# Optimization experiments

Hardware: AMD Instinct MI355X
Metric: run time of the kernel (lower is better)

Reference implementation:

```python
import jax, jax.numpy as jnp
import numpy as np

N_S, N_C, N_L = 100000, 20000, 5000
E_U, E_T = 2000000, 500000
D_S, D_C, D_L, H = 64, 32, 128, 128
N_LAYERS = 3  # num_layers=2 -> ModuleList holds 3 hetero layers


def _sage(h_src, h_dst, src_idx, dst_idx, W_self, W_neigh, b, n_dst):
    # DGL SAGEConv 'mean': fc_self(h_dst) + fc_neigh(mean of in-neighbor src feats) + bias
    summed = jax.ops.segment_sum(h_src[src_idx], dst_idx, num_segments=n_dst)  # [n_dst, d]
    deg = jax.ops.segment_sum(jnp.ones((src_idx.shape[0],), h_src.dtype), dst_idx, num_segments=n_dst)
    h_neigh = summed / jnp.maximum(deg, 1.0)[:, None]
    return h_dst @ W_self + h_neigh @ W_neigh + b


def setup_inputs() -> dict:
    key = jax.random.key(0)
    ks = jax.random.split(key, 24)
    s = 0.05
    inp = {
        'feat_student': jax.random.normal(ks[0], (N_S, D_S), jnp.float32),
        'feat_concept': jax.random.normal(ks[1], (N_C, D_C), jnp.float32),
        'feat_lecture': jax.random.normal(ks[2], (N_L, D_L), jnp.float32),
        'W_fs': jax.random.normal(ks[3], (D_S, H), jnp.float32) * s,
        'b_fs': jnp.zeros((H,), jnp.float32),
        'W_fc': jax.random.normal(ks[4], (D_C, H), jnp.float32) * s,
        'b_fc': jnp.zeros((H,), jnp.float32),
        'W_fl': jax.random.normal(ks[5], (D_L, H), jnp.float32) * s,
        'b_fl': jnp.zeros((H,), jnp.float32),
        # per-layer, per-relation SAGE params (all dims 128 so they stack)
        'W_self_u': jax.random.normal(ks[6], (N_LAYERS, H, H), jnp.float32) * s,
        'W_neigh_u': jax.random.normal(ks[7], (N_LAYERS, H, H), jnp.float32) * s,
        'b_u': jnp.zeros((N_LAYERS, H), jnp.float32),
        'W_self_t': jax.random.normal(ks[8], (N_LAYERS, H, H), jnp.float32) * s,
        'W_neigh_t': jax.random.normal(ks[9], (N_LAYERS, H, H), jnp.float32) * s,
        'b_t': jnp.zeros((N_LAYERS, H), jnp.float32),
        'und_src': jax.random.randint(ks[10], (E_U,), 0, N_S, jnp.int32),
        'und_dst': jax.random.randint(ks[11], (E_U,), 0, N_C, jnp.int32),
        'tea_src': jax.random.randint(ks[12], (E_T,), 0, N_L, jnp.int32),
        'tea_dst': jax.random.randint(ks[13], (E_T,), 0, N_C, jnp.int32),
    }
    return inp


def reference(feat_student, feat_concept, feat_lecture,
              W_fs, b_fs, W_fc, b_fc, W_fl, b_fl,
              W_self_u, W_neigh_u, b_u, W_self_t, W_neigh_t, b_t,
              und_src, und_dst, tea_src, tea_dst):
    # input projections per node type
    h_s = feat_student @ W_fs + b_fs
    h_c = feat_concept @ W_fc + b_fc
    h_l = feat_lecture @ W_fl + b_fl
    n_c = h_c.shape[0]
    for i in range(N_LAYERS):
        ou = _sage(h_s, h_c, und_src, und_dst, W_self_u[i], W_neigh_u[i], b_u[i], n_c)
        ot = _sage(h_l, h_c, tea_src, tea_dst, W_self_t[i], W_neigh_t[i], b_t[i], n_c)
        # HeteroGraphConv cross-relation aggregate: 'mean' on layer 0, default 'sum' after
        h_c = (ou + ot) * (0.5 if i == 0 else 1.0)
        if i != N_LAYERS - 1:
            h_c = jax.nn.relu(h_c)  # dropout is identity in eval mode
        # student/lecture are never destination types -> features pass through
    return h_c  # [N_C, 128] concept embeddings
```

## Files before the change

### kernel.cpp

```cpp
#include <hip/hip_runtime.h>
#include <hip/hip_bf16.h>
#include <cstdint>
#include <cstddef>

#define NS_ 100000
#define NC_ 20000
#define NL_ 5000
#define EU_ 2000000
#define ET_ 500000
#define H_  128

#define NBK_ 625
#define CHK_ 3908
#define UBLK_ 512
#define TBLK_ 128
#define CAPU_ 3600
#define CAPT_ 1024
#define SEDGE_ 3712

typedef __attribute__((ext_vector_type(8))) short bs8;
typedef __attribute__((ext_vector_type(4))) float f32x4;
typedef __attribute__((ext_vector_type(2))) float v2f;

__device__ inline short bf_rne(float f) {
    unsigned u = __float_as_uint(f);
    u = (u + 0x7fffu + ((u >> 16) & 1u)) >> 16;
    return (short)u;
}
__device__ inline unsigned pack_bf16x2(float a, float b) {
    return ((unsigned)(unsigned short)bf_rne(a)) |
           (((unsigned)(unsigned short)bf_rne(b)) << 16);
}
__device__ inline float bflo(unsigned w) { return __uint_as_float(w << 16); }
__device__ inline float bfhi(unsigned w) { return __uint_as_float(w & 0xffff0000u); }

#define B_SCU UBLK_
#define B_SCT TBLK_
#define B_CVT 512
#define B_PACK 480
#define B_BC 2
#define B_WFC 16
#define B_TOTAL (B_SCU + B_SCT + B_CVT + B_PACK + B_BC + B_WFC)

__global__ __launch_bounds__(256) void prep_fused_kernel(
    const int* __restrict__ und_dst, const int* __restrict__ und_src,
    const int* __restrict__ tea_dst, const int* __restrict__ tea_src,
    unsigned* __restrict__ gcurU, unsigned* __restrict__ gcurT,
    unsigned* __restrict__ binnedU, unsigned* __restrict__ binnedT,
    const float* __restrict__ feat_s, unsigned* __restrict__ fs8,
    const float* __restrict__ feat_l, unsigned* __restrict__ flb,
    const float* __restrict__ Wsu, const float* __restrict__ Wnu,
    const float* __restrict__ Wst, const float* __restrict__ Wnt,
    const float* __restrict__ W_fs, const float* __restrict__ W_fl,
    short* __restrict__ WpL,
    const float* __restrict__ bu, const float* __restrict__ bt,
    const float* __restrict__ b_fs, const float* __restrict__ b_fl,
    float* __restrict__ bc,
    const float* __restrict__ W_fc, short* __restrict__ WpC)
{
    __shared__ unsigned smem[9476];
    const int b = blockIdx.x;
    const int tid = threadIdx.x;

    if (b < B_SCU + B_SCT) {
        const bool isU = (b < B_SCU);
        const int blk = isU ? b : (b - B_SCU);
        const int nEdge = isU ? EU_ : ET_;
        const int* dstp = isU ? und_dst : tea_dst;
        const int* srcp = isU ? und_src : tea_src;
        unsigned* gcur = isU ? gcurU : gcurT;
        unsigned* binned = isU ? binnedU : binnedT;
        const unsigned cap = isU ? CAPU_ : CAPT_;
        unsigned* sed  = smem;
        unsigned* sed2 = smem + 3968;
        unsigned* cnt  = smem + 7936;
        unsigned* pre  = smem + 8704;
        unsigned* wsum = smem + 9472;
        for (int i = tid; i < 768; i += 256) cnt[i] = 0;
        __syncthreads();
        const int start = blk * CHK_;
        const int end = min(start + CHK_, nEdge);
        const int n = end - start;
        const int n4 = n >> 2;
        const int4* d4 = (const int4*)(dstp + start);
        const int4* s4 = (const int4*)(srcp + start);
        for (int i = tid; i < n4; i += 256) {
            int4 dv = d4[i];
            int4 sv = s4[i];
            unsigned k0 = (unsigned)dv.x >> 5, k1 = (unsigned)dv.y >> 5;
            unsigned k2 = (unsigned)dv.z >> 5, k3 = (unsigned)dv.w >> 5;
            sed[4 * i + 0] = (unsigned)sv.x | ((unsigned)(dv.x & 31) << 17) | (k0 << 22);
            sed[4 * i + 1] = (unsigned)sv.y | ((unsigned)(dv.y & 31) << 17) | (k1 << 22);
            sed[4 * i + 2] = (unsigned)sv.z | ((unsigned)(dv.z & 31) << 17) | (k2 << 22);
            sed[4 * i + 3] = (unsigned)sv.w | ((unsigned)(dv.w & 31) << 17) | (k3 << 22);
            atomicAdd(&cnt[k0], 1u);
            atomicAdd(&cnt[k1], 1u);
            atomicAdd(&cnt[k2], 1u);
            atomicAdd(&cnt[k3], 1u);
        }
        for (int i = (n4 << 2) + tid; i < n; i += 256) {
            int d = dstp[start + i];
            unsigned k = (unsigned)d >> 5;
            sed[i] = (unsigned)srcp[start + i] | ((unsigned)(d & 31) << 17) | (k << 22);
            atomicAdd(&cnt[k], 1u);
        }
        __syncthreads();
        unsigned c0 = cnt[3 * tid], c1 = cnt[3 * tid + 1], c2 = cnt[3 * tid + 2];
        unsigned s = c0 + c1 + c2;
        const int lane = tid & 63;
        const int wv = tid >> 6;
        unsigned v = s;
#pragma unroll
        for (int d = 1; d < 64; d <<= 1) {
            unsigned t = __shfl_up(v, d, 64);
            if (lane >= d) v += t;
        }
        if (lane == 63) wsum[wv] = v;
        __syncthreads();
        unsigned wo = 0;
        for (int w = 0; w < wv; w++) wo += wsum[w];
        unsigned excl = v - s + wo;
        pre[3 * tid] = excl;
        pre[3 * tid + 1] = excl + c0;
        pre[3 * tid + 2] = excl + c0 + c1;
        __syncthreads();
        for (int k = tid; k < NBK_; k += 256) {
            unsigned L = cnt[k];
            unsigned W = L ? atomicAdd(&gcur[k], L) : 0;
            if (W + L > cap) W = cap - L;
            cnt[k] = k * cap + W - pre[k];
        }
        __syncthreads();
        for (int i = tid; i < n; i += 256) {
            unsigned e = sed[i];
            unsigned pos = atomicAdd(&pre[e >> 22], 1u);
            sed2[pos] = e;
        }
        __syncthreads();
        for (int i = tid; i < n; i += 256) {
            unsigned e = sed2[i];
            binned[cnt[e >> 22] + i] = e & 0x3FFFFFu;
        }
    } else if (b < B_SCU + B_SCT + B_CVT) {
        int i = (b - B_SCU - B_SCT) * 256 + tid;
        const int stride = B_CVT * 256;
        const int nS = NS_ * 16;
        const int nTot = nS + NL_ * 64;
        for (; i < nTot; i += stride) {
            if (i < nS) {
                const float4 v = ((const float4*)feat_s)[i];
                unsigned r = __builtin_amdgcn_cvt_pk_fp8_f32(v.x, v.y, 0, false);
                r = __builtin_amdgcn_cvt_pk_fp8_f32(v.z, v.w, r, true);
                fs8[i] = r;
            } else {
                int j = i - nS;
                float2 v = ((const float2*)feat_l)[j];
                flb[j] = pack_bf16x2(v.x, v.y);
            }
        }
    } else if (b < B_SCU + B_SCT + B_CVT + B_PACK) {
        int i = (b - B_SCU - B_SCT - B_CVT) * 256 + tid;
        int j = i & 7;
        int lane = (i >> 3) & 63;
        int nt = (i >> 9) & 7;
        int ktAll = i >> 12;
        int l = ktAll / 10;
        int kt = ktAll - l * 10;
        int k = kt * 32 + (lane >> 4) * 8 + j;
        int n = nt * 16 + (lane & 15);
        const size_t WL = (size_t)l * H_ * H_;
        float v;
        if (k < 128) {
            v = Wsu[WL + k * H_ + n] + Wst[WL + k * H_ + n];
        } else if (k < 192) {
            int a = k - 128;
            v = 0.f;
            for (int t = 0; t < 128; t++) v += W_fs[a * H_ + t] * Wnu[WL + t * H_ + n];
        } else {
            int a = k - 192;
            v = 0.f;
            for (int t = 0; t < 128; t++) v += W_fl[a * H_ + t] * Wnt[WL + t * H_ + n];
        }
        WpL[i] = bf_rne(v);
    } else if (b < B_SCU + B_SCT + B_CVT + B_PACK + B_BC) {
        int i = (b - B_SCU - B_SCT - B_CVT - B_PACK) * 256 + tid;
        if (i < 3 * H_) {
            int l = i >> 7, c = i & 127;
            const size_t WL = (size_t)l * H_ * H_;
            float v = bu[i] + bt[i];
            for (int j2 = 0; j2 < 128; j2++)
                v += b_fs[j2] * Wnu[WL + j2 * H_ + c] + b_fl[j2] * Wnt[WL + j2 * H_ + c];
            bc[i] = v;
        }
    } else {
        int i = (b - (B_SCU + B_SCT + B_CVT + B_PACK + B_BC)) * 256 + tid;
        int j = i & 7;
        int lane = (i >> 3) & 63;
        int nt = (i >> 9) & 7;
        int k = (lane >> 4) * 8 + j;
        int n = nt * 16 + (lane & 15);
        WpC[i] = bf_rne(W_fc[k * H_ + n]);
    }
}

__global__ __launch_bounds__(256) void agg_kernel(
    const unsigned* __restrict__ gcurU, const unsigned* __restrict__ binnedU,
    const uint2* __restrict__ fs8, unsigned* __restrict__ aggFu,
    const unsigned* __restrict__ gcurT, const unsigned* __restrict__ binnedT,
    const uint4* __restrict__ flb4, unsigned* __restrict__ aggFt)
{
    __shared__ unsigned sedA[SEDGE_];
    __shared__ unsigned sedB[SEDGE_];
    __shared__ unsigned sh[32], soff[33], scur[32];
    const int b = blockIdx.x;
    const int tid = threadIdx.x;
    const bool isU = (b < NBK_);
    const int bb = isU ? b : (b - NBK_);
    const unsigned* binned = isU ? binnedU : binnedT;
    const unsigned cap = isU ? CAPU_ : CAPT_;
    const unsigned* base = binned + (size_t)bb * cap;
    const int n = min((int)(isU ? gcurU : gcurT)[bb], (int)cap);

    if (tid < 32) sh[tid] = 0;
    __syncthreads();
    const int n4 = n >> 2;
    for (int i = tid; i < n4; i += 256) {
        uint4 w = ((const uint4*)base)[i];
        sedA[4 * i + 0] = w.x; atomicAdd(&sh[(w.x >> 17) & 31], 1u);
        sedA[4 * i + 1] = w.y; atomicAdd(&sh[(w.y >> 17) & 31], 1u);
        sedA[4 * i + 2] = w.z; atomicAdd(&sh[(w.z >> 17) & 31], 1u);
        sedA[4 * i + 3] = w.w; atomicAdd(&sh[(w.w >> 17) & 31], 1u);
    }
    for (int i = (n4 << 2) + tid; i < n; i += 256) {
        unsigned e = base[i];
        sedA[i] = e;
        atomicAdd(&sh[(e >> 17) & 31], 1u);
    }
    __syncthreads();
    if (tid == 0) {
        unsigned r = 0;
        for (int j = 0; j < 32; j++) {
            unsigned v = sh[j];
            soff[j] = r;
            scur[j] = r;
            r += v;
        }
        soff[32] = r;
    }
    __syncthreads();
    for (int i = tid; i < n; i += 256) {
        unsigned e = sedA[i];
        unsigned pos = atomicAdd(&scur[(e >> 17) & 31], 1u);
        if (pos < SEDGE_) sedB[pos] = e & 0x1FFFFu;
    }
    __syncthreads();

    const int g = tid >> 3;
    const int sub = tid & 7;
    const int gs = (int)soff[g];
    const int ge = (int)min(soff[g + 1], (unsigned)SEDGE_);
    const int c = bb * 32 + g;
    const float inv = 1.f / (float)max(ge - gs, 1);

    if (isU) {
        float a[8];
#pragma unroll
        for (int i = 0; i < 8; i++) a[i] = 0.f;
        int e = gs;
        for (; e + 2 <= ge; e += 2) {
            unsigned s0 = sedB[e], s1 = sedB[e + 1];
            uint2 w0 = fs8[(size_t)s0 * 8 + sub];
            uint2 w1 = fs8[(size_t)s1 * 8 + sub];
            v2f p0 = __builtin_amdgcn_cvt_pk_f32_fp8(w0.x, false);
            v2f p1 = __builtin_amdgcn_cvt_pk_f32_fp8(w0.x, true);
            v2f p2 = __builtin_amdgcn_cvt_pk_f32_fp8(w0.y, false);
            v2f p3 = __builtin_amdgcn_cvt_pk_f32_fp8(w0.y, true);
            a[0] += p0.x; a[1] += p0.y; a[2] += p1.x; a[3] += p1.y;
            a[4] += p2.x; a[5] += p2.y; a[6] += p3.x; a[7] += p3.y;
            p0 = __builtin_amdgcn_cvt_pk_f32_fp8(w1.x, false);
            p1 = __builtin_amdgcn_cvt_pk_f32_fp8(w1.x, true);
            p2 = __builtin_amdgcn_cvt_pk_f32_fp8(w1.y, false);
            p3 = __builtin_amdgcn_cvt_pk_f32_fp8(w1.y, true);
            a[0] += p0.x; a[1] += p0.y; a[2] += p1.x; a[3] += p1.y;
            a[4] += p2.x; a[5] += p2.y; a[6] += p3.x; a[7] += p3.y;
        }
        if (e < ge) {
            uint2 w0 = fs8[(size_t)sedB[e] * 8 + sub];
            v2f p0 = __builtin_amdgcn_cvt_pk_f32_fp8(w0.x, false);
            v2f p1 = __builtin_amdgcn_cvt_pk_f32_fp8(w0.x, true);
            v2f p2 = __builtin_amdgcn_cvt_pk_f32_fp8(w0.y, false);
            v2f p3 = __builtin_amdgcn_cvt_pk_f32_fp8(w0.y, true);
            a[0] += p0.x; a[1] += p0.y; a[2] += p1.x; a[3] += p1.y;
            a[4] += p2.x; a[5] += p2.y; a[6] += p3.x; a[7] += p3.y;
        }
        uint4 o;
        o.x = pack_bf16x2(a[0] * inv, a[1] * inv);
        o.y = pack_bf16x2(a[2] * inv, a[3] * inv);
        o.z = pack_bf16x2(a[4] * inv, a[5] * inv);
        o.w = pack_bf16x2(a[6] * inv, a[7] * inv);
        ((uint4*)aggFu)[(size_t)c * 8 + sub] = o;
    } else {
        float a[16];
#pragma unroll
        for (int i = 0; i < 16; i++) a[i] = 0.f;
        for (int e = gs; e < ge; e++) {
            unsigned src = sedB[e];
            uint4 w0 = flb4[(size_t)src * 16 + sub * 2];
            uint4 w1 = flb4[(size_t)src * 16 + sub * 2 + 1];
            a[0] += bflo(w0.x); a[1] += bfhi(w0.x);
            a[2] += bflo(w0.y); a[3] += bfhi(w0.y);
            a[4] += bflo(w0.z); a[5] += bfhi(w0.z);
            a[6] += bflo(w0.w); a[7] += bfhi(w0.w);
            a[8]  += bflo(w1.x); a[9]  += bfhi(w1.x);
            a[10] += bflo(w1.y); a[11] += bfhi(w1.y);
            a[12] += bflo(w1.z); a[13] += bfhi(w1.z);
            a[14] += bflo(w1.w); a[15] += bfhi(w1.w);
        }
        uint4 o0, o1;
        o0.x = pack_bf16x2(a[0] * inv, a[1] * inv);
        o0.y = pack_bf16x2(a[2] * inv, a[3] * inv);
        o0.z = pack_bf16x2(a[4] * inv, a[5] * inv);
        o0.w = pack_bf16x2(a[6] * inv, a[7] * inv);
        o1.x = pack_bf16x2(a[8] * inv, a[9] * inv);
        o1.y = pack_bf16x2(a[10] * inv, a[11] * inv);
        o1.z = pack_bf16x2(a[12] * inv, a[13] * inv);
        o1.w = pack_bf16x2(a[14] * inv, a[15] * inv);
        ((uint4*)aggFt)[(size_t)c * 16 + sub * 2] = o0;
        ((uint4*)aggFt)[(size_t)c * 16 + sub * 2 + 1] = o1;
    }
}

__global__ __launch_bounds__(256) void layers_fused_kernel(
    const float* __restrict__ feat_c, const short* __restrict__ WpC,
    const float* __restrict__ b_fc,
    const unsigned* __restrict__ aggFu, const unsigned* __restrict__ aggFt,
    const short* __restrict__ WpL, const float* __restrict__ bc,
    float* __restrict__ out)
{
    __shared__ short lds[4][16 * 132];
    const int tid = threadIdx.x;
    const int lane = tid & 63;
    const int wv = tid >> 6;
    const int row0 = blockIdx.x * 64 + wv * 16;
    const int q = lane >> 4;
    const int m = lane & 15;
    const int rA = min(row0 + m, NC_ - 1);
    short* tile = lds[wv];

    bs8 fuF[2], ftF[4], hcF[4];
#pragma unroll
    for (int kt = 0; kt < 2; kt++)
        fuF[kt] = *(const bs8*)(aggFu + (size_t)rA * 32 + kt * 16 + q * 4);
#pragma unroll
    for (int kt = 0; kt < 4; kt++)
        ftF[kt] = *(const bs8*)(aggFt + (size_t)rA * 64 + kt * 16 + q * 4);

    f32x4 acc[8];
#pragma unroll
    for (int i = 0; i < 8; i++) acc[i] = (f32x4){0.f, 0.f, 0.f, 0.f};
    {
        const float* xp = feat_c + (size_t)rA * 32 + q * 8;
        float4 xa = *(const float4*)xp;
        float4 xb = *(const float4*)(xp + 4);
        bs8 af;
        af[0] = bf_rne(xa.x); af[1] = bf_rne(xa.y); af[2] = bf_rne(xa.z); af[3] = bf_rne(xa.w);
        af[4] = bf_rne(xb.x); af[5] = bf_rne(xb.y); af[6] = bf_rne(xb.z); af[7] = bf_rne(xb.w);
#pragma unroll
        for (int nt = 0; nt < 8; nt++) {
            bs8 bfr = *(const bs8*)(WpC + ((size_t)nt * 64 + lane) * 8);
            acc[nt] = __builtin_amdgcn_mfma_f32_16x16x32_bf16(af, bfr, acc[nt], 0, 0, 0);
        }
    }
#pragma unroll
    for (int nt = 0; nt < 8; nt++) {
        int col = nt * 16 + m;
        float bv = b_fc[col];
#pragma unroll
        for (int r = 0; r < 4; r++)
            tile[(q * 4 + r) * 132 + col] = bf_rne(acc[nt][r] + bv);
    }
#pragma unroll
    for (int kt = 0; kt < 4; kt++)
        hcF[kt] = *(const bs8*)(tile + m * 132 + kt * 32 + q * 8);

#pragma unroll
    for (int l = 0; l < 3; l++) {
#pragma unroll
        for (int i = 0; i < 8; i++) acc[i] = (f32x4){0.f, 0.f, 0.f, 0.f};
        const short* wl = WpL + (size_t)l * 40960;
#pragma unroll
        for (int kt = 0; kt < 10; kt++) {
            bs8 af = (kt < 4) ? hcF[kt] : ((kt < 6) ? fuF[kt - 4] : ftF[kt - 6]);
            const short* wp = wl + (size_t)kt * 4096;
#pragma unroll
            for (int nt = 0; nt < 8; nt++) {
                bs8 bfr = *(const bs8*)(wp + ((size_t)nt * 64 + lane) * 8);
                acc[nt] = __builtin_amdgcn_mfma_f32_16x16x32_bf16(af, bfr, acc[nt], 0, 0, 0);
            }
        }
        const float scale = (l == 0) ? 0.5f : 1.0f;
        const float* bl = bc + l * H_;
        if (l < 2) {
#pragma unroll
            for (int nt = 0; nt < 8; nt++) {
                int col = nt * 16 + m;
                float bv = bl[col];
#pragma unroll
                for (int r = 0; r < 4; r++)
                    tile[(q * 4 + r) * 132 + col] =
                        bf_rne(fmaxf((acc[nt][r] + bv) * scale, 0.f));
            }
#pragma unroll
            for (int kt = 0; kt < 4; kt++)
                hcF[kt] = *(const bs8*)(tile + m * 132 + kt * 32 + q * 8);
        } else {
#pragma unroll
            for (int nt = 0; nt < 8; nt++) {
                int col = nt * 16 + m;
                float bv = bl[col];
#pragma unroll
                for (int r = 0; r < 4; r++) {
                    int row = row0 + q * 4 + r;
                    if (row < NC_)
                        out[(size_t)row * H_ + col] = (acc[nt][r] + bv) * scale;
                }
            }
        }
    }
}

extern "C" void kernel_launch(void* const* d_in, const int* in_sizes, int n_in,
                              void* d_out, int out_size, void* d_ws, size_t ws_size,
                              hipStream_t stream)
{
    (void)in_sizes; (void)n_in; (void)out_size; (void)ws_size;
    const float* feat_s = (const float*)d_in[0];
    const float* feat_c = (const float*)d_in[1];
    const float* feat_l = (const float*)d_in[2];
    const float* W_fs = (const float*)d_in[3];
    const float* b_fs = (const float*)d_in[4];
    const float* W_fc = (const float*)d_in[5];
    const float* b_fc = (const float*)d_in[6];
    const float* W_fl = (const float*)d_in[7];
    const float* b_fl = (const float*)d_in[8];
    const float* W_self_u  = (const float*)d_in[9];
    const float* W_neigh_u = (const float*)d_in[10];
    const float* b_u = (const float*)d_in[11];
    const float* W_self_t  = (const float*)d_in[12];
    const float* W_neigh_t = (const float*)d_in[13];
    const float* b_t = (const float*)d_in[14];
    const int* und_src = (const int*)d_in[15];
    const int* und_dst = (const int*)d_in[16];
    const int* tea_src = (const int*)d_in[17];
    const int* tea_dst = (const int*)d_in[18];
    float* out = (float*)d_out;

    char* ws = (char*)d_ws;
    size_t o = 0;
    auto alloc = [&](size_t bytes) -> char* {
        char* p = ws + o;
        o += (bytes + 255) & ~(size_t)255;
        return p;
    };
    unsigned* fs8  = (unsigned*)alloc((size_t)NS_ * 16 * 4);
    unsigned* flb  = (unsigned*)alloc((size_t)NL_ * 64 * 4);
    unsigned* aggFu = (unsigned*)alloc((size_t)NC_ * 32 * 4);
    unsigned* aggFt = (unsigned*)alloc((size_t)NC_ * 64 * 4);
    short* WpL = (short*)alloc((size_t)3 * 10 * 8 * 64 * 8 * 2);
    short* WpC = (short*)alloc((size_t)8 * 64 * 8 * 2);
    float* bc  = (float*)alloc((size_t)3 * H_ * 4);
    unsigned* gcurU = (unsigned*)alloc((size_t)NBK_ * 4);
    unsigned* gcurT = (unsigned*)alloc((size_t)NBK_ * 4);
    unsigned* binnedU = (unsigned*)alloc((size_t)NBK_ * CAPU_ * 4);
    unsigned* binnedT = (unsigned*)alloc((size_t)NBK_ * CAPT_ * 4);

    hipMemsetAsync(gcurU, 0, (size_t)((char*)binnedU - (char*)gcurU), stream);

    prep_fused_kernel<<<B_TOTAL, 256, 0, stream>>>(
        und_dst, und_src, tea_dst, tea_src, gcurU, gcurT, binnedU, binnedT,
        feat_s, fs8, feat_l, flb,
        W_self_u, W_neigh_u, W_self_t, W_neigh_t, W_fs, W_fl, WpL,
        b_u, b_t, b_fs, b_fl, bc,
        W_fc, WpC);

    agg_kernel<<<2 * NBK_, 256, 0, stream>>>(
        gcurU, binnedU, (const uint2*)fs8, aggFu,
        gcurT, binnedT, (const uint4*)flb, aggFt);

    layers_fused_kernel<<<(NC_ + 63) / 64, 256, 0, stream>>>(
        feat_c, WpC, b_fc, aggFu, aggFt, WpL, bc, out);
}
```

Before: 218.1 us.

## Fuse neighbor aggregation into layer kernel via shared-memory tiles per bucket

Merges the aggregation kernel and the three-layer MFMA kernel into one kernel with one block per 32-concept bucket. The block first aggregates the student and lecture relations and writes the results as bf16 into shared memory, then the matmul stage reads them from there. This removes the global aggFu/aggFt round trip and one launch. The MFMA work is split across four waves by row and column group, which adds block-wide syncs. The prep kernel's edge-chunk size is halved, which doubles the scatter blocks and shrinks their shared memory. The fused kernel launches only 625 blocks, so parallelism and latency hiding drop compared with the 1250 plus 313 blocks before.

```diff
diff --git a/kernel.cpp b/kernel.cpp
--- a/kernel.cpp
+++ b/kernel.cpp
@@ -11,9 +11,9 @@
 #define H_  128
 
 #define NBK_ 625
-#define CHK_ 3908
-#define UBLK_ 512
-#define TBLK_ 128
+#define CHK_ 1956
+#define UBLK_ 1023
+#define TBLK_ 256
 #define CAPU_ 3600
 #define CAPT_ 1024
 #define SEDGE_ 3712
@@ -58,7 +58,7 @@
     float* __restrict__ bc,
     const float* __restrict__ W_fc, short* __restrict__ WpC)
 {
-    __shared__ unsigned smem[9476];
+    __shared__ unsigned smem[5508];
     const int b = blockIdx.x;
     const int tid = threadIdx.x;
 
@@ -72,15 +72,15 @@
         unsigned* binned = isU ? binnedU : binnedT;
         const unsigned cap = isU ? CAPU_ : CAPT_;
         unsigned* sed  = smem;
-        unsigned* sed2 = smem + 3968;
-        unsigned* cnt  = smem + 7936;
-        unsigned* pre  = smem + 8704;
-        unsigned* wsum = smem + 9472;
+        unsigned* sed2 = smem + 1984;
+        unsigned* cnt  = smem + 3968;
+        unsigned* pre  = smem + 4736;
+        unsigned* wsum = smem + 5504;
         for (int i = tid; i < 768; i += 256) cnt[i] = 0;
         __syncthreads();
         const int start = blk * CHK_;
         const int end = min(start + CHK_, nEdge);
-        const int n = end - start;
+        const int n = max(end - start, 0);
         const int n4 = n >> 2;
         const int4* d4 = (const int4*)(dstp + start);
         const int4* s4 = (const int4*)(srcp + start);
@@ -203,24 +203,31 @@
     }
 }
 
-__global__ __launch_bounds__(256) void agg_kernel(
-    const unsigned* __restrict__ gcurU, const unsigned* __restrict__ binnedU,
-    const uint2* __restrict__ fs8, unsigned* __restrict__ aggFu,
-    const unsigned* __restrict__ gcurT, const unsigned* __restrict__ binnedT,
-    const uint4* __restrict__ flb4, unsigned* __restrict__ aggFt)
+#define SEDA_OFF 0
+#define SEDB_OFF SEDGE_
+#define TU_OFF   (2 * SEDGE_)
+#define TT_OFF   (TU_OFF + 32 * 36)
+#define SH_OFF   (TT_OFF + 32 * 68)
+#define SOFF_OFF (SH_OFF + 32)
+#define SCUR_OFF (SOFF_OFF + 33)
+#define SMEM_TOT (SCUR_OFF + 32)
+
+template <bool ISU>
+__device__ inline void agg_bucket(
+    int bb, const unsigned* __restrict__ gcur, const unsigned* __restrict__ binned,
+    const uint2* __restrict__ fs8, const uint4* __restrict__ flb4,
+    unsigned* __restrict__ smem, int tid)
 {
-    __shared__ unsigned sedA[SEDGE_];
-    __shared__ unsigned sedB[SEDGE_];
-    __shared__ unsigned sh[32], soff[33], scur[32];
-    const int b = blockIdx.x;
-    const int tid = threadIdx.x;
-    const bool isU = (b < NBK_);
-    const int bb = isU ? b : (b - NBK_);
-    const unsigned* binned = isU ? binnedU : binnedT;
-    const unsigned cap = isU ? CAPU_ : CAPT_;
+    unsigned* sedA = smem + SEDA_OFF;
+    unsigned* sedB = smem + SEDB_OFF;
+    unsigned* sh   = smem + SH_OFF;
+    unsigned* soff = smem + SOFF_OFF;
+    unsigned* scur = smem + SCUR_OFF;
+    const unsigned cap = ISU ? CAPU_ : CAPT_;
     const unsigned* base = binned + (size_t)bb * cap;
-    const int n = min((int)(isU ? gcurU : gcurT)[bb], (int)cap);
-
+    const int n = min((int)gcur[bb], (int)cap);
+
+    __syncthreads();
     if (tid < 32) sh[tid] = 0;
     __syncthreads();
     const int n4 = n >> 2;
@@ -259,10 +266,9 @@
     const int sub = tid & 7;
     const int gs = (int)soff[g];
     const int ge = (int)min(soff[g + 1], (unsigned)SEDGE_);
-    const int c = bb * 32 + g;
     const float inv = 1.f / (float)max(ge - gs, 1);
 
-    if (isU) {
+    if (ISU) {
         float a[8];
 #pragma unroll
         for (int i = 0; i < 8; i++) a[i] = 0.f;
@@ -293,12 +299,11 @@
             a[0] += p0.x; a[1] += p0.y; a[2] += p1.x; a[3] += p1.y;
             a[4] += p2.x; a[5] += p2.y; a[6] += p3.x; a[7] += p3.y;
         }
-        uint4 o;
-        o.x = pack_bf16x2(a[0] * inv, a[1] * inv);
-        o.y = pack_bf16x2(a[2] * inv, a[3] * inv);
-        o.z = pack_bf16x2(a[4] * inv, a[5] * inv);
-        o.w = pack_bf16x2(a[6] * inv, a[7] * inv);
-        ((uint4*)aggFu)[(size_t)c * 8 + sub] = o;
+        unsigned* tu = smem + TU_OFF + g * 36 + sub * 4;
+        tu[0] = pack_bf16x2(a[0] * inv, a[1] * inv);
+        tu[1] = pack_bf16x2(a[2] * inv, a[3] * inv);
+        tu[2] = pack_bf16x2(a[4] * inv, a[5] * inv);
+        tu[3] = pack_bf16x2(a[6] * inv, a[7] * inv);
     } else {
         float a[16];
 #pragma unroll
@@ -316,69 +321,77 @@
             a[12] += bflo(w1.z); a[13] += bfhi(w1.z);
             a[14] += bflo(w1.w); a[15] += bfhi(w1.w);
         }
-        uint4 o0, o1;
-        o0.x = pack_bf16x2(a[0] * inv, a[1] * inv);
-        o0.y = pack_bf16x2(a[2] * inv, a[3] * inv);
-        o0.z = pack_bf16x2(a[4] * inv, a[5] * inv);
-        o0.w = pack_bf16x2(a[6] * inv, a[7] * inv);
-        o1.x = pack_bf16x2(a[8] * inv, a[9] * inv);
-        o1.y = pack_bf16x2(a[10] * inv, a[11] * inv);
-        o1.z = pack_bf16x2(a[12] * inv, a[13] * inv);
-        o1.w = pack_bf16x2(a[14] * inv, a[15] * inv);
-        ((uint4*)aggFt)[(size_t)c * 16 + sub * 2] = o0;
-        ((uint4*)aggFt)[(size_t)c * 16 + sub * 2 + 1] = o1;
+        unsigned* tt = smem + TT_OFF + g * 68 + sub * 8;
+#pragma unroll
+        for (int i = 0; i < 8; i++)
+            tt[i] = pack_bf16x2(a[2 * i] * inv, a[2 * i + 1] * inv);
     }
 }
 
-__global__ __launch_bounds__(256) void layers_fused_kernel(
+__global__ __launch_bounds__(256) void agg_layers_kernel(
+    const unsigned* __restrict__ gcurU, const unsigned* __restrict__ binnedU,
+    const uint2* __restrict__ fs8,
+    const unsigned* __restrict__ gcurT, const unsigned* __restrict__ binnedT,
+    const uint4* __restrict__ flb4,
     const float* __restrict__ feat_c, const short* __restrict__ WpC,
     const float* __restrict__ b_fc,
-    const unsigned* __restrict__ aggFu, const unsigned* __restrict__ aggFt,
     const short* __restrict__ WpL, const float* __restrict__ bc,
     float* __restrict__ out)
 {
-    __shared__ short lds[4][16 * 132];
+    __shared__ unsigned smem[SMEM_TOT];
+    const int bb = blockIdx.x;
     const int tid = threadIdx.x;
+
+    agg_bucket<true>(bb, gcurU, binnedU, fs8, flb4, smem, tid);
+    agg_bucket<false>(bb, gcurT, binnedT, fs8, flb4, smem, tid);
+    __syncthreads();
+
     const int lane = tid & 63;
     const int wv = tid >> 6;
-    const int row0 = blockIdx.x * 64 + wv * 16;
+    const int rowgrp = wv & 1;
+    const int colgrp = wv >> 1;
     const int q = lane >> 4;
     const int m = lane & 15;
-    const int rA = min(row0 + m, NC_ - 1);
-    short* tile = lds[wv];
+    const int rloc = rowgrp * 16 + m;
+    const int row = bb * 32 + rloc;
 
     bs8 fuF[2], ftF[4], hcF[4];
 #pragma unroll
     for (int kt = 0; kt < 2; kt++)
-        fuF[kt] = *(const bs8*)(aggFu + (size_t)rA * 32 + kt * 16 + q * 4);
+        fuF[kt] = *(const bs8*)(smem + TU_OFF + rloc * 36 + kt * 16 + q * 4);
 #pragma unroll
     for (int kt = 0; kt < 4; kt++)
-        ftF[kt] = *(const bs8*)(aggFt + (size_t)rA * 64 + kt * 16 + q * 4);
-
-    f32x4 acc[8];
-#pragma unroll
-    for (int i = 0; i < 8; i++) acc[i] = (f32x4){0.f, 0.f, 0.f, 0.f};
+        ftF[kt] = *(const bs8*)(smem + TT_OFF + rloc * 68 + kt * 16 + q * 4);
+
+    short* tile = (short*)smem + rowgrp * 2112;
+
+    f32x4 acc[4];
+#pragma unroll
+    for (int i = 0; i < 4; i++) acc[i] = (f32x4){0.f, 0.f, 0.f, 0.f};
     {
-        const float* xp = feat_c + (size_t)rA * 32 + q * 8;
+        const float* xp = feat_c + (size_t)row * 32 + q * 8;
         float4 xa = *(const float4*)xp;
         float4 xb = *(const float4*)(xp + 4);
         bs8 af;
         af[0] = bf_rne(xa.x); af[1] = bf_rne(xa.y); af[2] = bf_rne(xa.z); af[3] = bf_rne(xa.w);
         af[4] = bf_rne(xb.x); af[5] = bf_rne(xb.y); af[6] = bf_rne(xb.z); af[7] = bf_rne(xb.w);
 #pragma unroll
-        for (int nt = 0; nt < 8; nt++) {
+        for (int j = 0; j < 4; j++) {
+            int nt = colgrp * 4 + j;
             bs8 bfr = *(const bs8*)(WpC + ((size_t)nt * 64 + lane) * 8);
-            acc[nt] = __builtin_amdgcn_mfma_f32_16x16x32_bf16(af, bfr, acc[nt], 0, 0, 0);
-        }
-    }
-#pragma unroll
-    for (int nt = 0; nt < 8; nt++) {
-        int col = nt * 16 + m;
+            acc[j] = __builtin_amdgcn_mfma_f32_16x16x32_bf16(af, bfr, acc[j], 0, 0, 0);
+        }
+    }
+    __syncthreads();
+#pragma unroll
+    for (int j = 0; j < 4; j++) {
+        int col = (colgrp * 4 + j) * 16 + m;
         float bv = b_fc[col];
 #pragma unroll
         for (int r = 0; r < 4; r++)
-            tile[(q * 4 + r) * 132 + col] = bf_rne(acc[nt][r] + bv);
-    }
+            tile[(q * 4 + r) * 132 + col] = bf_rne(acc[j][r] + bv);
+    }
+    __syncthreads();
 #pragma unroll
     for (int kt = 0; kt < 4; kt++)
         hcF[kt] = *(const bs8*)(tile + m * 132 + kt * 32 + q * 8);
@@ -386,43 +399,45 @@
 #pragma unroll
     for (int l = 0; l < 3; l++) {
 #pragma unroll
-        for (int i = 0; i < 8; i++) acc[i] = (f32x4){0.f, 0.f, 0.f, 0.f};
+        for (int i = 0; i < 4; i++) acc[i] = (f32x4){0.f, 0.f, 0.f, 0.f};
         const short* wl = WpL + (size_t)l * 40960;
 #pragma unroll
         for (int kt = 0; kt < 10; kt++) {
             bs8 af = (kt < 4) ? hcF[kt] : ((kt < 6) ? fuF[kt - 4] : ftF[kt - 6]);
             const short* wp = wl + (size_t)kt * 4096;
 #pragma unroll
-            for (int nt = 0; nt < 8; nt++) {
+            for (int j = 0; j < 4; j++) {
+                int nt = colgrp * 4 + j;
                 bs8 bfr = *(const bs8*)(wp + ((size_t)nt * 64 + lane) * 8);
-                acc[nt] = __builtin_amdgcn_mfma_f32_16x16x32_bf16(af, bfr, acc[nt], 0, 0, 0);
+                acc[j] = __builtin_amdgcn_mfma_f32_16x16x32_bf16(af, bfr, acc[j], 0, 0, 0);
             }
         }
         const float scale = (l == 0) ? 0.5f : 1.0f;
         const float* bl = bc + l * H_;
         if (l < 2) {
-#pragma unroll
-            for (int nt = 0; nt < 8; nt++) {
-                int col = nt * 16 + m;
+            __syncthreads();
+#pragma unroll
+            for (int j = 0; j < 4; j++) {
+                int col = (colgrp * 4 + j) * 16 + m;
                 float bv = bl[col];
 #pragma unroll
                 for (int r = 0; r < 4; r++)
                     tile[(q * 4 + r) * 132 + col] =
-                        bf_rne(fmaxf((acc[nt][r] + bv) * scale, 0.f));
+                        bf_rne(fmaxf((acc[j][r] + bv) * scale, 0.f));
             }
+            __syncthreads();
 #pragma unroll
             for (int kt = 0; kt < 4; kt++)
                 hcF[kt] = *(const bs8*)(tile + m * 132 + kt * 32 + q * 8);
         } else {
 #pragma unroll
-            for (int nt = 0; nt < 8; nt++) {
-                int col = nt * 16 + m;
+            for (int j = 0; j < 4; j++) {
+                int col = (colgrp * 4 + j) * 16 + m;
                 float bv = bl[col];
 #pragma unroll
                 for (int r = 0; r < 4; r++) {
-                    int row = row0 + q * 4 + r;
-                    if (row < NC_)
-                        out[(size_t)row * H_ + col] = (acc[nt][r] + bv) * scale;
+                    int orow = bb * 32 + rowgrp * 16 + q * 4 + r;
+                    out[(size_t)orow * H_ + col] = (acc[j][r] + bv) * scale;
                 }
             }
         }
@@ -464,8 +479,6 @@
     };
     unsigned* fs8  = (unsigned*)alloc((size_t)NS_ * 16 * 4);
     unsigned* flb  = (unsigned*)alloc((size_t)NL_ * 64 * 4);
-    unsigned* aggFu = (unsigned*)alloc((size_t)NC_ * 32 * 4);
-    unsigned* aggFt = (unsigned*)alloc((size_t)NC_ * 64 * 4);
     short* WpL = (short*)alloc((size_t)3 * 10 * 8 * 64 * 8 * 2);
     short* WpC = (short*)alloc((size_t)8 * 64 * 8 * 2);
     float* bc  = (float*)alloc((size_t)3 * H_ * 4);
@@ -483,10 +496,8 @@
         b_u, b_t, b_fs, b_fl, bc,
         W_fc, WpC);
 
-    agg_kernel<<<2 * NBK_, 256, 0, stream>>>(
-        gcurU, binnedU, (const uint2*)fs8, aggFu,
-        gcurT, binnedT, (const uint4*)flb, aggFt);
-
-    layers_fused_kernel<<<(NC_ + 63) / 64, 256, 0, stream>>>(
-        feat_c, WpC, b_fc, aggFu, aggFt, WpL, bc, out);
+    agg_layers_kernel<<<NBK_, 256, 0, stream>>>(
+        gcurU, binnedU, (const uint2*)fs8,
+        gcurT, binnedT, (const uint4*)flb,
+        feat_c, WpC, b_fc, WpL, bc, out);
 }
```

After: 227.2 us. 1.04x slower.
